# Kernel optimization log

Hardware: AMD Instinct MI355X
Metric: run time of the kernel (lower is better)

Reference implementation:

```python
import jax, jax.numpy as jnp
import numpy as np

B = 1048576  # number of particles


def setup_inputs() -> dict:
    key = jax.random.key(0)
    kF, = jax.random.split(key, 1)
    # near-identity deformation gradients: positive det, distinct singular values
    F = jnp.eye(3, dtype=jnp.float32) + 0.1 * jax.random.normal(kF, (B, 3, 3), dtype=jnp.float32)
    return {
        "F": F,
        "youngs_modulus_log": jnp.asarray(11.5, dtype=jnp.float32),
        "poissons_ratio": jnp.asarray(0.3, dtype=jnp.float32),
        "yield_stress": jnp.asarray(1000.0, dtype=jnp.float32),
        "alpha": jnp.asarray(0.3, dtype=jnp.float32),
        "cohesion": jnp.asarray(0.0, dtype=jnp.float32),
    }


def _recompose(U, sigma, Vh):
    # U @ diag(sigma) @ Vh without materializing diag matrices
    return jnp.einsum('bij,bj,bjk->bik', U, sigma, Vh)


def reference(F, youngs_modulus_log, poissons_ratio, yield_stress, alpha, cohesion):
    E = jnp.exp(youngs_modulus_log)
    nu = poissons_ratio
    mu = E / (2.0 * (1.0 + nu))
    la = E * nu / ((1.0 + nu) * (1.0 - 2.0 * nu))

    # single batched 3x3 SVD shared by plasticine and sand branches
    U, s, Vh = jnp.linalg.svd(F)  # (B,3,3), (B,3), (B,3,3)

    # ---- plasticine (von Mises return mapping) ----
    s_p = jnp.maximum(s, 0.01)
    eps = jnp.log(s_p)                              # (B,3)
    tr = jnp.sum(eps, axis=1, keepdims=True)
    eps_bar = eps - tr / 3.0
    eps_bar_norm = jnp.linalg.norm(eps_bar, axis=1, keepdims=True) + 1e-5
    delta_gamma = eps_bar_norm - yield_stress / (2.0 * mu)
    yield_eps = eps - delta_gamma / eps_bar_norm * eps_bar
    sigma_plast = jnp.where(delta_gamma > 0, jnp.exp(yield_eps), s_p)
    F_plasticine = _recompose(U, sigma_plast, Vh)

    # ---- sand (Drucker-Prager return mapping) ----
    s_s = jnp.maximum(s, 0.05)
    eps_s = jnp.log(s_s)
    tr_s = jnp.sum(eps_s, axis=1, keepdims=True)
    eps_hat = eps_s - tr_s / 3.0
    eps_hat_norm = jnp.linalg.norm(eps_hat, axis=1, keepdims=True)
    expand_eps = jnp.full_like(eps_s, 1.0) * cohesion
    shifted_trace = tr_s - cohesion * 3.0
    cond_yield = shifted_trace < 0
    dg = eps_hat_norm + (3.0 * la + 2.0 * mu) / (2.0 * mu) * shifted_trace * alpha
    compress_eps = eps_s - jnp.maximum(dg, 0.0) / eps_hat_norm * eps_hat
    eps_final = jnp.where(cond_yield, compress_eps, expand_eps)
    F_sand = _recompose(U, jnp.exp(eps_final), Vh)

    # ---- water (volume-preserving projection) ----
    J = jnp.linalg.det(F)                            # (B,)
    Je_1_3 = jnp.power(J, 1.0 / 3.0)[:, None]        # (B,1)
    F_water = Je_1_3[:, :, None] * jnp.eye(3, dtype=F.dtype)  # diag(Je^{1/3}) per batch

    return 0.5 * F_plasticine + 0.3 * F_sand + 0.2 * F_water
```

## Files before the change

kernel.cpp:

```cpp
#include <hip/hip_runtime.h>
#include <hip/hip_bf16.h>

#define FRCP(x)  __builtin_amdgcn_rcpf(x)
#define FSQRT(x) __builtin_amdgcn_sqrtf(x)
#define FRSQ(x)  __builtin_amdgcn_rsqf(x)
#define FLOG2(x) __builtin_amdgcn_logf(x)
#define FEXP2(x) __builtin_amdgcn_exp2f(x)

__global__ __launch_bounds__(256) void physics_svd_kernel(
    const float* __restrict__ gF,
    const float* __restrict__ p_Elog,
    const float* __restrict__ p_nu,
    const float* __restrict__ p_ys,
    const float* __restrict__ p_alpha,
    const float* __restrict__ p_coh,
    float* __restrict__ gOut,
    int B)
{
    __shared__ __align__(16) float lds[2304];

    const int tid   = threadIdx.x;
    const int pbase = blockIdx.x * 256;
    const int nhere = min(256, B - pbase);
    const int nflt  = nhere * 9;

    if (nhere == 256) {
        const float4* g4 = reinterpret_cast<const float4*>(gF + (size_t)pbase * 9);
        float4* l4 = reinterpret_cast<float4*>(lds);
        l4[tid]       = g4[tid];
        l4[tid + 256] = g4[tid + 256];
        if (tid < 64) l4[tid + 512] = g4[tid + 512];
    } else {
        for (int j = tid; j < nflt; j += 256) lds[j] = gF[(size_t)pbase * 9 + j];
    }
    __syncthreads();

    const float E  = __expf(p_Elog[0]);
    const float nu = p_nu[0];
    const float ys = p_ys[0];
    const float al = p_alpha[0];
    const float co = p_coh[0];
    const float mu = E / (2.0f * (1.0f + nu));
    const float la = E * nu / ((1.0f + nu) * (1.0f - 2.0f * nu));
    const float ys_2mu = ys / (2.0f * mu);
    const float kk     = (3.0f * la + 2.0f * mu) / (2.0f * mu) * al;
    const float exp_co = __expf(co);

    if (tid < nhere) {
        float f[9];
        #pragma unroll
        for (int k = 0; k < 9; ++k) f[k] = lds[tid * 9 + k];

        float a00 = f[0]*f[0] + f[3]*f[3] + f[6]*f[6];
        float a01 = f[0]*f[1] + f[3]*f[4] + f[6]*f[7];
        float a02 = f[0]*f[2] + f[3]*f[5] + f[6]*f[8];
        float a11 = f[1]*f[1] + f[4]*f[4] + f[7]*f[7];
        float a12 = f[1]*f[2] + f[4]*f[5] + f[7]*f[8];
        float a22 = f[2]*f[2] + f[5]*f[5] + f[8]*f[8];

        float v00=1.f, v01=0.f, v02=0.f;
        float v10=0.f, v11=1.f, v12=0.f;
        float v20=0.f, v21=0.f, v22=1.f;

        #define JROT(APP, AQQ, APQ, RP, RQ, VP0, VQ0, VP1, VQ1, VP2, VQ2)             \
        {                                                                             \
            float apq = APQ;                                                          \
            float d   = AQQ - APP;                                                    \
            float p2  = apq + apq;                                                    \
            float h   = FSQRT(__builtin_fmaf(d, d, p2 * p2));                         \
            float w_  = FRCP(fabsf(d) + h);                                           \
            float t   = p2 * copysignf(w_, d);                                        \
            t = (apq == 0.0f) ? 0.0f : t;              \
            float c = FRSQ(__builtin_fmaf(t, t, 1.0f));                               \
            float s = t * c;                                                          \
            APP -= t * apq;  AQQ += t * apq;  APQ = 0.0f;                             \
            float pk = RP, qk = RQ;                                                   \
            RP = c*pk - s*qk;  RQ = s*pk + c*qk;                                      \
            float tmp;                                                                \
            tmp = VP0; VP0 = c*tmp - s*VQ0; VQ0 = s*tmp + c*VQ0;                      \
            tmp = VP1; VP1 = c*tmp - s*VQ1; VQ1 = s*tmp + c*VQ1;                      \
            tmp = VP2; VP2 = c*tmp - s*VQ2; VQ2 = s*tmp + c*VQ2;                      \
        }

        #pragma unroll
        for (int sweep = 0; sweep < 3; ++sweep) {
            JROT(a00, a11, a01, a02, a12, v00, v01, v10, v11, v20, v21)
            JROT(a00, a22, a02, a01, a12, v00, v02, v10, v12, v20, v22)
            JROT(a11, a22, a12, a01, a02, v01, v02, v11, v12, v21, v22)
        }
        #undef JROT

        a00 = fmaxf(a00, 0.0f);
        a11 = fmaxf(a11, 0.0f);
        a22 = fmaxf(a22, 0.0f);

        const float LN2_HALF = 0.34657359f;
        float e0 = LN2_HALF * FLOG2(fmaxf(a00, 1e-4f));
        float e1 = LN2_HALF * FLOG2(fmaxf(a11, 1e-4f));
        float e2 = LN2_HALF * FLOG2(fmaxf(a22, 1e-4f));

        const float HLOG = -2.9957323f;
        float h0 = (a00 >= 2.5e-3f) ? e0 : HLOG;
        float h1 = (a11 >= 2.5e-3f) ? e1 : HLOG;
        float h2 = (a22 >= 2.5e-3f) ? e2 : HLOG;

        const float INV_LN2 = 1.4426950f;
        float tr3 = (e0 + e1 + e2) * (1.0f/3.0f);
        float b0 = e0 - tr3, b1 = e1 - tr3, b2 = e2 - tr3;
        float bn = FSQRT(b0*b0 + b1*b1 + b2*b2) + 1e-5f;
        float rp = fmaxf(bn - ys_2mu, 0.0f) * FRCP(bn);
        float gp0 = FEXP2((e0 - rp*b0) * INV_LN2);
        float gp1 = FEXP2((e1 - rp*b1) * INV_LN2);
        float gp2 = FEXP2((e2 - rp*b2) * INV_LN2);

        float trs = h0 + h1 + h2;
        float t3  = trs * (1.0f/3.0f);
        float hb0 = h0 - t3, hb1 = h1 - t3, hb2 = h2 - t3;
        float hn = FSQRT(hb0*hb0 + hb1*hb1 + hb2*hb2);
        float st = trs - 3.0f * co;
        bool cond = st < 0.0f;
        float dg = hn + kk * st;
        float rs = fmaxf(dg, 0.0f) * FRCP(hn);
        float gs0 = cond ? FEXP2((h0 - rs*hb0) * INV_LN2) : exp_co;
        float gs1 = cond ? FEXP2((h1 - rs*hb1) * INV_LN2) : exp_co;
        float gs2 = cond ? FEXP2((h2 - rs*hb2) * INV_LN2) : exp_co;

        float w0 = (0.5f*gp0 + 0.3f*gs0) * FRSQ(a00);
        float w1 = (0.5f*gp1 + 0.3f*gs1) * FRSQ(a11);
        float w2 = (0.5f*gp2 + 0.3f*gs2) * FRSQ(a22);

        float J = f[0]*(f[4]*f[8] - f[5]*f[7])
                - f[1]*(f[3]*f[8] - f[5]*f[6])
                + f[2]*(f[3]*f[7] - f[4]*f[6]);
        float wd = 0.2f * FEXP2(FLOG2(J) * (1.0f/3.0f));

        float t00 = (f[0]*v00 + f[1]*v10 + f[2]*v20) * w0;
        float t01 = (f[0]*v01 + f[1]*v11 + f[2]*v21) * w1;
        float t02 = (f[0]*v02 + f[1]*v12 + f[2]*v22) * w2;
        float t10 = (f[3]*v00 + f[4]*v10 + f[5]*v20) * w0;
        float t11 = (f[3]*v01 + f[4]*v11 + f[5]*v21) * w1;
        float t12 = (f[3]*v02 + f[4]*v12 + f[5]*v22) * w2;
        float t20 = (f[6]*v00 + f[7]*v10 + f[8]*v20) * w0;
        float t21 = (f[6]*v01 + f[7]*v11 + f[8]*v21) * w1;
        float t22 = (f[6]*v02 + f[7]*v12 + f[8]*v22) * w2;

        float o[9];
        o[0] = t00*v00 + t01*v01 + t02*v02 + wd;
        o[1] = t00*v10 + t01*v11 + t02*v12;
        o[2] = t00*v20 + t01*v21 + t02*v22;
        o[3] = t10*v00 + t11*v01 + t12*v02;
        o[4] = t10*v10 + t11*v11 + t12*v12 + wd;
        o[5] = t10*v20 + t11*v21 + t12*v22;
        o[6] = t20*v00 + t21*v01 + t22*v02;
        o[7] = t20*v10 + t21*v11 + t22*v12;
        o[8] = t20*v20 + t21*v21 + t22*v22 + wd;

        #pragma unroll
        for (int k = 0; k < 9; ++k) lds[tid * 9 + k] = o[k];
    }
    __syncthreads();

    if (nhere == 256) {
        float4* g4 = reinterpret_cast<float4*>(gOut + (size_t)pbase * 9);
        const float4* l4 = reinterpret_cast<const float4*>(lds);
        g4[tid]       = l4[tid];
        g4[tid + 256] = l4[tid + 256];
        if (tid < 64) g4[tid + 512] = l4[tid + 512];
    } else {
        for (int j = tid; j < nflt; j += 256)
            gOut[(size_t)pbase * 9 + j] = lds[j];
    }
}

extern "C" void kernel_launch(void* const* d_in, const int* in_sizes, int n_in,
                              void* d_out, int out_size, void* d_ws, size_t ws_size,
                              hipStream_t stream) {
    const float* F      = (const float*)d_in[0];
    const float* p_Elog = (const float*)d_in[1];
    const float* p_nu   = (const float*)d_in[2];
    const float* p_ys   = (const float*)d_in[3];
    const float* p_al   = (const float*)d_in[4];
    const float* p_co   = (const float*)d_in[5];
    float* out = (float*)d_out;

    const int B = in_sizes[0] / 9;
    const int nblocks = (B + 255) / 256;
    physics_svd_kernel<<<nblocks, 256, 0, stream>>>(
        F, p_Elog, p_nu, p_ys, p_al, p_co, out, B);
}
```

Measured before the change: 106.8 us.

## Replace eigenvector tracking with spectral-function interpolation of F^T F

Drops the accumulation of Jacobi rotations into V and rebuilds the spectral weight matrix W = V diag(w) V^T as a quadratic polynomial in B = F^T F, fitted by Lagrange/Newton interpolation through the three eigenvalues. The output becomes F·W, which removes the 9-element V updates per rotation and the two 3x3 recomposition products. It also works in the log2 domain to fold the sigma^-1 factor into the exponentials. The risk is numerical: divided differences become ill-conditioned when eigenvalues are nearly equal, guarded only by a 1e-6 floor.

```diff
diff --git a/kernel.cpp b/kernel.cpp
--- a/kernel.cpp
+++ b/kernel.cpp
@@ -44,25 +44,28 @@
     const float la = E * nu / ((1.0f + nu) * (1.0f - 2.0f * nu));
     const float ys_2mu = ys / (2.0f * mu);
     const float kk     = (3.0f * la + 2.0f * mu) / (2.0f * mu) * al;
-    const float exp_co = __expf(co);
+    const float lco2   = co * 1.4426950f;
+
+    const float LN2      = 0.69314718f;
+    const float L2_1EM4  = -13.287712f;
+    const float L2_25EM4 = -8.6438562f;
 
     if (tid < nhere) {
         float f[9];
         #pragma unroll
         for (int k = 0; k < 9; ++k) f[k] = lds[tid * 9 + k];
 
-        float a00 = f[0]*f[0] + f[3]*f[3] + f[6]*f[6];
-        float a01 = f[0]*f[1] + f[3]*f[4] + f[6]*f[7];
-        float a02 = f[0]*f[2] + f[3]*f[5] + f[6]*f[8];
-        float a11 = f[1]*f[1] + f[4]*f[4] + f[7]*f[7];
-        float a12 = f[1]*f[2] + f[4]*f[5] + f[7]*f[8];
-        float a22 = f[2]*f[2] + f[5]*f[5] + f[8]*f[8];
+        float b00 = f[0]*f[0] + f[3]*f[3] + f[6]*f[6];
+        float b01 = f[0]*f[1] + f[3]*f[4] + f[6]*f[7];
+        float b02 = f[0]*f[2] + f[3]*f[5] + f[6]*f[8];
+        float b11 = f[1]*f[1] + f[4]*f[4] + f[7]*f[7];
+        float b12 = f[1]*f[2] + f[4]*f[5] + f[7]*f[8];
+        float b22 = f[2]*f[2] + f[5]*f[5] + f[8]*f[8];
 
-        float v00=1.f, v01=0.f, v02=0.f;
-        float v10=0.f, v11=1.f, v12=0.f;
-        float v20=0.f, v21=0.f, v22=1.f;
+        float a00 = b00, a01 = b01, a02 = b02;
+        float a11 = b11, a12 = b12, a22 = b22;
 
-        #define JROT(APP, AQQ, APQ, RP, RQ, VP0, VQ0, VP1, VQ1, VP2, VQ2)             \
+        #define JROT(APP, AQQ, APQ, RP, RQ)                                           \
         {                                                                             \
             float apq = APQ;                                                          \
             float d   = AQQ - APP;                                                    \
@@ -76,84 +79,86 @@
             APP -= t * apq;  AQQ += t * apq;  APQ = 0.0f;                             \
             float pk = RP, qk = RQ;                                                   \
             RP = c*pk - s*qk;  RQ = s*pk + c*qk;                                      \
-            float tmp;                                                                \
-            tmp = VP0; VP0 = c*tmp - s*VQ0; VQ0 = s*tmp + c*VQ0;                      \
-            tmp = VP1; VP1 = c*tmp - s*VQ1; VQ1 = s*tmp + c*VQ1;                      \
-            tmp = VP2; VP2 = c*tmp - s*VQ2; VQ2 = s*tmp + c*VQ2;                      \
         }
 
         #pragma unroll
         for (int sweep = 0; sweep < 3; ++sweep) {
-            JROT(a00, a11, a01, a02, a12, v00, v01, v10, v11, v20, v21)
-            JROT(a00, a22, a02, a01, a12, v00, v02, v10, v12, v20, v22)
-            JROT(a11, a22, a12, a01, a02, v01, v02, v11, v12, v21, v22)
+            JROT(a00, a11, a01, a02, a12)
+            JROT(a00, a22, a02, a01, a12)
+            JROT(a11, a22, a12, a01, a02)
         }
         #undef JROT
 
-        a00 = fmaxf(a00, 0.0f);
-        a11 = fmaxf(a11, 0.0f);
-        a22 = fmaxf(a22, 0.0f);
+        float l0 = fmaxf(a00, 1e-20f);
+        float l1 = fmaxf(a11, 1e-20f);
+        float l2 = fmaxf(a22, 1e-20f);
+        float li0 = FLOG2(l0), li1 = FLOG2(l1), li2 = FLOG2(l2);
 
-        const float LN2_HALF = 0.34657359f;
-        float e0 = LN2_HALF * FLOG2(fmaxf(a00, 1e-4f));
-        float e1 = LN2_HALF * FLOG2(fmaxf(a11, 1e-4f));
-        float e2 = LN2_HALF * FLOG2(fmaxf(a22, 1e-4f));
+        float p0 = 0.5f * fmaxf(li0, L2_1EM4);
+        float p1 = 0.5f * fmaxf(li1, L2_1EM4);
+        float p2 = 0.5f * fmaxf(li2, L2_1EM4);
+        float mp = (p0 + p1 + p2) * (1.0f/3.0f);
+        float bb0 = p0 - mp, bb1 = p1 - mp, bb2 = p2 - mp;
+        float bn = LN2 * FSQRT(bb0*bb0 + bb1*bb1 + bb2*bb2) + 1e-5f;
+        float rp = fmaxf(bn - ys_2mu, 0.0f) * FRCP(bn);
 
-        const float HLOG = -2.9957323f;
-        float h0 = (a00 >= 2.5e-3f) ? e0 : HLOG;
-        float h1 = (a11 >= 2.5e-3f) ? e1 : HLOG;
-        float h2 = (a22 >= 2.5e-3f) ? e2 : HLOG;
+        float q0 = 0.5f * fmaxf(li0, L2_25EM4);
+        float q1 = 0.5f * fmaxf(li1, L2_25EM4);
+        float q2 = 0.5f * fmaxf(li2, L2_25EM4);
+        float mq = (q0 + q1 + q2) * (1.0f/3.0f);
+        float hb0 = q0 - mq, hb1 = q1 - mq, hb2 = q2 - mq;
+        float hn = LN2 * FSQRT(hb0*hb0 + hb1*hb1 + hb2*hb2);
+        float st = LN2 * (q0 + q1 + q2) - 3.0f * co;
+        bool cond = st < 0.0f;
+        float rs = fmaxf(hn + kk * st, 0.0f) * FRCP(fmaxf(hn, 1e-20f));
 
-        const float INV_LN2 = 1.4426950f;
-        float tr3 = (e0 + e1 + e2) * (1.0f/3.0f);
-        float b0 = e0 - tr3, b1 = e1 - tr3, b2 = e2 - tr3;
-        float bn = FSQRT(b0*b0 + b1*b1 + b2*b2) + 1e-5f;
-        float rp = fmaxf(bn - ys_2mu, 0.0f) * FRCP(bn);
-        float gp0 = FEXP2((e0 - rp*b0) * INV_LN2);
-        float gp1 = FEXP2((e1 - rp*b1) * INV_LN2);
-        float gp2 = FEXP2((e2 - rp*b2) * INV_LN2);
+        float hl0 = 0.5f * li0, hl1 = 0.5f * li1, hl2 = 0.5f * li2;
+        float w0 = 0.5f * FEXP2(p0 - rp*bb0 - hl0)
+                 + 0.3f * FEXP2(cond ? (q0 - rs*hb0 - hl0) : (lco2 - hl0));
+        float w1 = 0.5f * FEXP2(p1 - rp*bb1 - hl1)
+                 + 0.3f * FEXP2(cond ? (q1 - rs*hb1 - hl1) : (lco2 - hl1));
+        float w2 = 0.5f * FEXP2(p2 - rp*bb2 - hl2)
+                 + 0.3f * FEXP2(cond ? (q2 - rs*hb2 - hl2) : (lco2 - hl2));
 
-        float trs = h0 + h1 + h2;
-        float t3  = trs * (1.0f/3.0f);
-        float hb0 = h0 - t3, hb1 = h1 - t3, hb2 = h2 - t3;
-        float hn = FSQRT(hb0*hb0 + hb1*hb1 + hb2*hb2);
-        float st = trs - 3.0f * co;
-        bool cond = st < 0.0f;
-        float dg = hn + kk * st;
-        float rs = fmaxf(dg, 0.0f) * FRCP(hn);
-        float gs0 = cond ? FEXP2((h0 - rs*hb0) * INV_LN2) : exp_co;
-        float gs1 = cond ? FEXP2((h1 - rs*hb1) * INV_LN2) : exp_co;
-        float gs2 = cond ? FEXP2((h2 - rs*hb2) * INV_LN2) : exp_co;
+        float d10 = l1 - l0, d21 = l2 - l1, d20 = l2 - l0;
+        float i10 = FRCP(copysignf(fmaxf(fabsf(d10), 1e-6f), d10));
+        float i21 = FRCP(copysignf(fmaxf(fabsf(d21), 1e-6f), d21));
+        float i20 = FRCP(copysignf(fmaxf(fabsf(d20), 1e-6f), d20));
+        float c1  = (w1 - w0) * i10;
+        float w12 = (w2 - w1) * i21;
+        float c2  = (w12 - c1) * i20;
+        float beta  = c1 - c2 * (l0 + l1);
+        float alpha = w0 - c1 * l0 + c2 * l0 * l1;
 
-        float w0 = (0.5f*gp0 + 0.3f*gs0) * FRSQ(a00);
-        float w1 = (0.5f*gp1 + 0.3f*gs1) * FRSQ(a11);
-        float w2 = (0.5f*gp2 + 0.3f*gs2) * FRSQ(a22);
+        float s00 = b00*b00 + b01*b01 + b02*b02;
+        float s01 = b00*b01 + b01*b11 + b02*b12;
+        float s02 = b00*b02 + b01*b12 + b02*b22;
+        float s11 = b01*b01 + b11*b11 + b12*b12;
+        float s12 = b01*b02 + b11*b12 + b12*b22;
+        float s22 = b02*b02 + b12*b12 + b22*b22;
+
+        float W00 = c2*s00 + beta*b00 + alpha;
+        float W01 = c2*s01 + beta*b01;
+        float W02 = c2*s02 + beta*b02;
+        float W11 = c2*s11 + beta*b11 + alpha;
+        float W12 = c2*s12 + beta*b12;
+        float W22 = c2*s22 + beta*b22 + alpha;
 
         float J = f[0]*(f[4]*f[8] - f[5]*f[7])
                 - f[1]*(f[3]*f[8] - f[5]*f[6])
                 + f[2]*(f[3]*f[7] - f[4]*f[6]);
         float wd = 0.2f * FEXP2(FLOG2(J) * (1.0f/3.0f));
 
-        float t00 = (f[0]*v00 + f[1]*v10 + f[2]*v20) * w0;
-        float t01 = (f[0]*v01 + f[1]*v11 + f[2]*v21) * w1;
-        float t02 = (f[0]*v02 + f[1]*v12 + f[2]*v22) * w2;
-        float t10 = (f[3]*v00 + f[4]*v10 + f[5]*v20) * w0;
-        float t11 = (f[3]*v01 + f[4]*v11 + f[5]*v21) * w1;
-        float t12 = (f[3]*v02 + f[4]*v12 + f[5]*v22) * w2;
-        float t20 = (f[6]*v00 + f[7]*v10 + f[8]*v20) * w0;
-        float t21 = (f[6]*v01 + f[7]*v11 + f[8]*v21) * w1;
-        float t22 = (f[6]*v02 + f[7]*v12 + f[8]*v22) * w2;
-
         float o[9];
-        o[0] = t00*v00 + t01*v01 + t02*v02 + wd;
-        o[1] = t00*v10 + t01*v11 + t02*v12;
-        o[2] = t00*v20 + t01*v21 + t02*v22;
-        o[3] = t10*v00 + t11*v01 + t12*v02;
-        o[4] = t10*v10 + t11*v11 + t12*v12 + wd;
-        o[5] = t10*v20 + t11*v21 + t12*v22;
-        o[6] = t20*v00 + t21*v01 + t22*v02;
-        o[7] = t20*v10 + t21*v11 + t22*v12;
-        o[8] = t20*v20 + t21*v21 + t22*v22 + wd;
+        o[0] = f[0]*W00 + f[1]*W01 + f[2]*W02 + wd;
+        o[1] = f[0]*W01 + f[1]*W11 + f[2]*W12;
+        o[2] = f[0]*W02 + f[1]*W12 + f[2]*W22;
+        o[3] = f[3]*W00 + f[4]*W01 + f[5]*W02;
+        o[4] = f[3]*W01 + f[4]*W11 + f[5]*W12 + wd;
+        o[5] = f[3]*W02 + f[4]*W12 + f[5]*W22;
+        o[6] = f[6]*W00 + f[7]*W01 + f[8]*W02;
+        o[7] = f[6]*W01 + f[7]*W11 + f[8]*W12;
+        o[8] = f[6]*W02 + f[7]*W12 + f[8]*W22 + wd;
 
         #pragma unroll
         for (int k = 0; k < 9; ++k) lds[tid * 9 + k] = o[k];
```

Result: faster. 102.1 us (-4.4%).
